# Optimization experiments

Measured on AMD Instinct MI355X. Metric: run time of the kernel, lower is better.

## Reference

```python
import jax, jax.numpy as jnp
import numpy as np

B, T, C, H = 4, 2048, 1024, 16
HD = C // H  # head dim = 64


def setup_inputs() -> dict:
    key = jax.random.key(0)
    k1, k2, k3, k4, k5 = jax.random.split(key, 5)
    s_in = 1.0 / np.sqrt(C)
    return {
        "x": jax.random.normal(k1, (B, T, C), dtype=jnp.float32),
        "W_attn": jax.random.uniform(k2, (C, 3 * C), dtype=jnp.float32, minval=-s_in, maxval=s_in),
        "b_attn": jax.random.uniform(k3, (3 * C,), dtype=jnp.float32, minval=-s_in, maxval=s_in),
        "W_proj": jax.random.uniform(k4, (C, C), dtype=jnp.float32, minval=-s_in, maxval=s_in),
        "b_proj": jax.random.uniform(k5, (C,), dtype=jnp.float32, minval=-s_in, maxval=s_in),
    }


def reference(x, W_attn, b_attn, W_proj, b_proj):
    Bx, Tx, Cx = x.shape
    qkv = x @ W_attn + b_attn                      # [B,T,3C]
    q, k, v = jnp.split(qkv, 3, axis=2)
    # [B,T,C] -> [B,H,T,HD]
    def heads(t):
        return t.reshape(Bx, Tx, H, HD).transpose(0, 2, 1, 3)
    q, k, v = heads(q), heads(k), heads(v)
    scale = 1.0 / np.sqrt(HD).astype(np.float32)
    att = jnp.einsum('bhqd,bhkd->bhqk', q, k) * scale
    causal = jnp.tril(jnp.ones((Tx, Tx), dtype=bool))
    att = jnp.where(causal[None, None], att, -jnp.inf)
    att = jax.nn.softmax(att, axis=-1)
    y = jnp.einsum('bhqk,bhkd->bhqd', att, v)      # [B,H,T,HD]
    y = y.transpose(0, 2, 1, 3).reshape(Bx, Tx, Cx)
    return y @ W_proj + b_proj
```

## Files before the change

kernel.cpp:

```cpp
#include <hip/hip_runtime.h>
#include <math.h>

#define Bn 4
#define Tn 2048
#define Cn 1024
#define Hn 16
#define HDn 64
#define Mn (Bn * Tn)

typedef unsigned short u16;
typedef unsigned int u32;
typedef __attribute__((ext_vector_type(8))) short bf16x8;
typedef __attribute__((ext_vector_type(8))) unsigned short us8;
typedef __attribute__((ext_vector_type(4))) float f32x4;
typedef __attribute__((ext_vector_type(16))) float f32x16;
typedef __attribute__((ext_vector_type(4))) unsigned int u32x4;

__device__ __forceinline__ float b2f(u16 u) {
    return __uint_as_float(((u32)u) << 16);
}
__device__ __forceinline__ u16 f2b(float f) {
    u32 u = __float_as_uint(f);
    return (u16)((u + 0x7FFFu + ((u >> 16) & 1u)) >> 16);
}
__device__ __forceinline__ u32 cvtpk(float a, float b) {
    u32 d;
    asm("v_cvt_pk_bf16_f32 %0, %1, %2" : "=v"(d) : "v"(a), "v"(b));
    return d;
}
__device__ __forceinline__ void pswap(u32& a, u32& b) {
    asm("v_permlane32_swap_b32 %0, %1" : "+v"(a), "+v"(b));
}

__device__ __forceinline__ int xcd_work(int bid, int nwg) {
    return (bid & 7) * (nwg >> 3) + (bid >> 3);
}

#define GLL(srcp, dstp)                                                     \
    __builtin_amdgcn_global_load_lds(                                       \
        (const __attribute__((address_space(1))) u32*)(srcp),               \
        (__attribute__((address_space(3))) u32*)(dstp), 16, 0, 0)

#define WAITCNT6() asm volatile("s_waitcnt vmcnt(6)" ::: "memory")
#define WAITCNT4() asm volatile("s_waitcnt vmcnt(4)" ::: "memory")
#define WAITCNT0() asm volatile("s_waitcnt vmcnt(0)" ::: "memory")

__global__ __launch_bounds__(256) void cvt_f32_bf16_kernel(
    const float4* __restrict__ in, ushort4* __restrict__ out, int n4)
{
    for (int i = blockIdx.x * 256 + threadIdx.x; i < n4; i += gridDim.x * 256) {
        float4 v = in[i];
        ushort4 o;
        o.x = f2b(v.x); o.y = f2b(v.y); o.z = f2b(v.z); o.w = f2b(v.w);
        out[i] = o;
    }
}

__global__ __launch_bounds__(256) void transpose_cvt_kernel(
    const float* __restrict__ in, u16* __restrict__ out, int R, int Cc)
{
    __shared__ u16 t[32][33];
    const int c0 = blockIdx.x * 32, r0 = blockIdx.y * 32;
    const int tx = threadIdx.x & 31, ty = threadIdx.x >> 5;
    #pragma unroll
    for (int i = 0; i < 32; i += 8)
        t[ty + i][tx] = f2b(in[(size_t)(r0 + ty + i) * Cc + c0 + tx]);
    __syncthreads();
    #pragma unroll
    for (int i = 0; i < 32; i += 8)
        out[(size_t)(c0 + ty + i) * R + r0 + tx] = t[tx][ty + i];
}

template <bool OUT_BF16, bool QKV_MODE>
__global__ __launch_bounds__(256, 2) void gemm_bf16_kernel(
    const u16* __restrict__ A, const u16* __restrict__ BT,
    const float* __restrict__ bias,
    u16* __restrict__ outb, float* __restrict__ outf, u16* __restrict__ vTout,
    int N, int K, int nx)
{
    __shared__ u16 Al[3][128 * 32];
    __shared__ u16 Bl[3][256 * 32];

    const int tid = threadIdx.x;
    const int workid = xcd_work(blockIdx.x, gridDim.x);
    const int brow = (workid / nx) * 128;
    const int bcol = (workid % nx) * 256;
    const int w  = tid >> 6;
    const int wr = w >> 1, wc = w & 1;
    const int l  = tid & 63;
    const int lr = l & 15;
    const int lk = (l >> 4) << 3;

    const int sr = l >> 2;
    const int sc = (l & 3) << 3;

    f32x4 acc[4][8];
    #pragma unroll
    for (int m = 0; m < 4; ++m)
        #pragma unroll
        for (int n = 0; n < 8; ++n) acc[m][n] = (f32x4){0.f, 0.f, 0.f, 0.f};

    #define STAGE_G(k0, bufi)                                                   \
        do {                                                                    \
            GLL(&A [(size_t)(brow + 32 * w +      sr) * K + (k0) + sc],         \
                &Al[bufi][(32 * w) * 32]);                                      \
            GLL(&A [(size_t)(brow + 32 * w + 16 + sr) * K + (k0) + sc],         \
                &Al[bufi][(32 * w + 16) * 32]);                                 \
            GLL(&BT[(size_t)(bcol + 64 * w +      sr) * K + (k0) + sc],         \
                &Bl[bufi][(64 * w) * 32]);                                      \
            GLL(&BT[(size_t)(bcol + 64 * w + 16 + sr) * K + (k0) + sc],         \
                &Bl[bufi][(64 * w + 16) * 32]);                                 \
            GLL(&BT[(size_t)(bcol + 64 * w + 32 + sr) * K + (k0) + sc],         \
                &Bl[bufi][(64 * w + 32) * 32]);                                 \
            GLL(&BT[(size_t)(bcol + 64 * w + 48 + sr) * K + (k0) + sc],         \
                &Bl[bufi][(64 * w + 48) * 32]);                                 \
        } while (0)

    const int T = K >> 5;
    STAGE_G(0, 0);
    STAGE_G(32, 1);

    int cur = 0;
    for (int t = 0; t < T; ++t) {
        if (t < T - 1) WAITCNT6();
        else           WAITCNT0();
        __builtin_amdgcn_s_barrier();

        if (t + 2 < T) {
            const int nb = cur + 2 >= 3 ? cur - 1 : cur + 2;
            STAGE_G((t + 2) << 5, nb);
        }

        bf16x8 a[4], b[8];
        #pragma unroll
        for (int m = 0; m < 4; ++m)
            a[m] = *(const bf16x8*)&Al[cur][(wr * 64 + m * 16 + lr) * 32 + lk];
        #pragma unroll
        for (int n = 0; n < 8; ++n)
            b[n] = *(const bf16x8*)&Bl[cur][(wc * 128 + n * 16 + lr) * 32 + lk];

        __builtin_amdgcn_s_setprio(1);
        #pragma unroll
        for (int m = 0; m < 4; ++m)
            #pragma unroll
            for (int n = 0; n < 8; ++n)
                acc[m][n] = __builtin_amdgcn_mfma_f32_16x16x32_bf16(
                    a[m], b[n], acc[m][n], 0, 0, 0);
        __builtin_amdgcn_s_setprio(0);

        cur = cur == 2 ? 0 : cur + 1;
    }
    #undef STAGE_G

    const int orow0 = brow + wr * 64 + ((l >> 4) << 2);
    const int ocol0 = bcol + wc * 128 + lr;
    if (QKV_MODE && bcol >= 2048) {
        #pragma unroll
        for (int n = 0; n < 8; ++n) {
            const int c = ocol0 + n * 16 - 2048;
            const float bv = bias[ocol0 + n * 16];
            #pragma unroll
            for (int m = 0; m < 4; ++m) {
                const int row0 = orow0 + m * 16;
                const int bb = row0 >> 11, t0 = row0 & 2047;
                ushort4 pk;
                pk.x = f2b(acc[m][n][0] + bv);
                pk.y = f2b(acc[m][n][1] + bv);
                pk.z = f2b(acc[m][n][2] + bv);
                pk.w = f2b(acc[m][n][3] + bv);
                *(ushort4*)&vTout[((size_t)bb * Cn + c) * Tn + t0] = pk;
            }
        }
    } else {
        #pragma unroll
        for (int n = 0; n < 8; ++n) {
            const int col = ocol0 + n * 16;
            const float bv = bias[col];
            #pragma unroll
            for (int m = 0; m < 4; ++m) {
                #pragma unroll
                for (int r = 0; r < 4; ++r) {
                    const int row = orow0 + m * 16 + r;
                    const float v = acc[m][n][r] + bv;
                    if (OUT_BF16) outb[(size_t)row * N + col] = f2b(v);
                    else          outf[(size_t)row * N + col] = v;
                }
            }
        }
    }
}

__global__ __launch_bounds__(256, 2) void attn_mfma7_kernel(
    const u16* __restrict__ qkvb, const u16* __restrict__ vT,
    u16* __restrict__ yb)
{
    __shared__ u16 Kb[3][64 * 64];
    __shared__ u16 Vb[3][64 * 64];

    const int tid = threadIdx.x;
    const int w   = tid >> 6;
    const int l   = tid & 63;
    const int q31 = l & 31;
    const int hi  = l >> 5;
    const int work = xcd_work(blockIdx.x, 512);
    const int pr  = work & 7;
    const int bh  = work >> 3;
    const int b   = bh >> 4, h = bh & 15;

    const float S2 = 0.18033688f;

    const u16* Kg = qkvb + (size_t)(b * Tn) * (3 * Cn) + Cn + h * HDn;
    const u16* Vg = vT + (size_t)bh * HDn * Tn;

    const int srow = l >> 3;
    const int schk = ((l & 7) ^ srow) << 3;
    const int rloc = w * 16;
    const int rsw8 = q31 & 7;

    #define STAGE_A(kt, bufi)                                                  \
        do {                                                                   \
            _Pragma("unroll")                                                  \
            for (int jc = 0; jc < 2; ++jc) {                                   \
                const int rr = rloc + jc * 8;                                  \
                GLL(Kg + (size_t)((kt) * 64 + rr + srow) * (3 * Cn) + schk,    \
                    &Kb[bufi][rr * 64]);                                       \
                GLL(Vg + (size_t)(rr + srow) * Tn + (kt) * 64 + schk,          \
                    &Vb[bufi][rr * 64]);                                       \
            }                                                                  \
        } while (0)

    #pragma unroll 1
    for (int half = 0; half < 2; ++half) {
        const int qt = half ? (15 - pr) : pr;
        const int ktmax = 2 * qt + 2;
        const int qrow0 = qt * 128 + w * 32;
        const int qglob = qrow0 + q31;

        const u16* Qp = qkvb + (size_t)(b * Tn + qglob) * (3 * Cn)
                        + h * HDn + hi * 8;
        bf16x8 qf[4];
        #pragma unroll
        for (int c = 0; c < 4; ++c) qf[c] = *(const bf16x8*)(Qp + c * 16);

        f32x16 O0, O1;
        #pragma unroll
        for (int r = 0; r < 16; ++r) { O0[r] = 0.f; O1[r] = 0.f; }
        float m = -INFINITY, ls = 0.f;

        STAGE_A(0, 0);
        STAGE_A(1, 1);

        int cur = 0;
        for (int kt = 0; kt < ktmax; ++kt) {
            if (kt < ktmax - 1) WAITCNT4();
            else                WAITCNT0();
            __builtin_amdgcn_s_barrier();

            if (kt + 2 < ktmax) {
                const int nb = cur + 2 >= 3 ? cur - 1 : cur + 2;
                STAGE_A(kt + 2, nb);
            }
            const u16* Kc = Kb[cur];
            const u16* Vc = Vb[cur];

            if (kt * 64 <= qrow0 + 31) {
                f32x16 S0, S1;
                #pragma unroll
                for (int r = 0; r < 16; ++r) { S0[r] = 0.f; S1[r] = 0.f; }
                __builtin_amdgcn_s_setprio(1);
                #pragma unroll
                for (int c = 0; c < 4; ++c) {
                    const int co = ((2 * c + hi) ^ rsw8) << 3;
                    const bf16x8 k0 = *(const bf16x8*)&Kc[q31 * 64 + co];
                    const bf16x8 k1 = *(const bf16x8*)&Kc[(32 + q31) * 64 + co];
                    S0 = __builtin_amdgcn_mfma_f32_32x32x16_bf16(k0, qf[c], S0, 0, 0, 0);
                    S1 = __builtin_amdgcn_mfma_f32_32x32x16_bf16(k1, qf[c], S1, 0, 0, 0);
                }
                __builtin_amdgcn_s_setprio(0);

                if (kt * 64 + 63 > qrow0) {
                    #pragma unroll
                    for (int r = 0; r < 16; ++r) {
                        const int kl = kt * 64 + (r & 3) + 8 * (r >> 2) + 4 * hi;
                        if (kl > qglob)      S0[r] = -INFINITY;
                        if (kl + 32 > qglob) S1[r] = -INFINITY;
                    }
                }

                float mt = S0[0];
                #pragma unroll
                for (int r = 1; r < 16; ++r) mt = fmaxf(mt, S0[r]);
                #pragma unroll
                for (int r = 0; r < 16; ++r) mt = fmaxf(mt, S1[r]);
                mt = fmaxf(mt, __shfl_xor(mt, 32));

                float lscale = 1.f;
                if (__any(mt > m + 64.f)) {
                    const float mn = fmaxf(m, mt);
                    const float alpha = exp2f((m - mn) * S2);
                    m = mn; lscale = alpha;
                    #pragma unroll
                    for (int r = 0; r < 16; ++r) {
                        const int qloc = (r & 3) + 8 * (r >> 2) + 4 * hi;
                        const float ar = __shfl(alpha, qloc);
                        O0[r] *= ar; O1[r] *= ar;
                    }
                }

                float lt = 0.f;
                u32 w0[8], w1[8];
                #pragma unroll
                for (int i = 0; i < 8; ++i) {
                    const float p0 = exp2f((S0[2 * i]     - m) * S2);
                    const float p1 = exp2f((S0[2 * i + 1] - m) * S2);
                    const float p2 = exp2f((S1[2 * i]     - m) * S2);
                    const float p3 = exp2f((S1[2 * i + 1] - m) * S2);
                    lt += (p0 + p1) + (p2 + p3);
                    w0[i] = cvtpk(p0, p1);
                    w1[i] = cvtpk(p2, p3);
                }
                lt += __shfl_xor(lt, 32);
                ls = ls * lscale + lt;

                __builtin_amdgcn_s_setprio(1);
                #pragma unroll
                for (int t2 = 0; t2 < 2; ++t2) {
                    #pragma unroll
                    for (int c1 = 0; c1 < 2; ++c1) {
                        u32 a0 = t2 ? w1[4 * c1 + 0] : w0[4 * c1 + 0];
                        u32 b0 = t2 ? w1[4 * c1 + 2] : w0[4 * c1 + 2];
                        u32 a1 = t2 ? w1[4 * c1 + 1] : w0[4 * c1 + 1];
                        u32 b1 = t2 ? w1[4 * c1 + 3] : w0[4 * c1 + 3];
                        pswap(a0, b0);
                        pswap(a1, b1);
                        u32x4 fr; fr.x = a0; fr.y = a1; fr.z = b0; fr.w = b1;
                        const bf16x8 pf = __builtin_bit_cast(bf16x8, fr);
                        const int c = t2 * 2 + c1;
                        const int co = ((2 * c + hi) ^ rsw8) << 3;
                        const bf16x8 v0 = *(const bf16x8*)&Vc[q31 * 64 + co];
                        const bf16x8 v1 = *(const bf16x8*)&Vc[(32 + q31) * 64 + co];
                        O0 = __builtin_amdgcn_mfma_f32_32x32x16_bf16(pf, v0, O0, 0, 0, 0);
                        O1 = __builtin_amdgcn_mfma_f32_32x32x16_bf16(pf, v1, O1, 0, 0, 0);
                    }
                }
                __builtin_amdgcn_s_setprio(0);
            }

            cur = cur == 2 ? 0 : cur + 1;
        }

        __builtin_amdgcn_s_barrier();

        #pragma unroll
        for (int r = 0; r < 16; ++r) {
            const int qloc = (r & 3) + 8 * (r >> 2) + 4 * hi;
            const float inv = __builtin_amdgcn_rcpf(__shfl(ls, qloc));
            u16* yp = yb + (size_t)(b * Tn + qrow0 + qloc) * Cn + h * HDn + q31;
            yp[0]  = f2b(O0[r] * inv);
            yp[32] = f2b(O1[r] * inv);
        }
    }
    #undef STAGE_A
}

extern "C" void kernel_launch(void* const* d_in, const int* in_sizes, int n_in,
                              void* d_out, int out_size, void* d_ws, size_t ws_size,
                              hipStream_t stream)
{
    const float* x      = (const float*)d_in[0];
    const float* W_attn = (const float*)d_in[1];
    const float* b_attn = (const float*)d_in[2];
    const float* W_proj = (const float*)d_in[3];
    const float* b_proj = (const float*)d_in[4];
    float* out = (float*)d_out;

    u16* xb   = (u16*)d_ws;
    u16* WaT  = xb   + (size_t)Mn * Cn;
    u16* WpT  = WaT  + (size_t)3 * Cn * Cn;
    u16* qkvb = WpT  + (size_t)Cn * Cn;
    u16* yb   = qkvb + (size_t)Mn * 3 * Cn;
    u16* vT   = yb   + (size_t)Mn * Cn;

    cvt_f32_bf16_kernel<<<2048, 256, 0, stream>>>(
        (const float4*)x, (ushort4*)xb, Mn * Cn / 4);

    transpose_cvt_kernel<<<dim3(3 * Cn / 32, Cn / 32), 256, 0, stream>>>(
        W_attn, WaT, Cn, 3 * Cn);
    transpose_cvt_kernel<<<dim3(Cn / 32, Cn / 32), 256, 0, stream>>>(
        W_proj, WpT, Cn, Cn);

    gemm_bf16_kernel<true, true><<<64 * 12, 256, 0, stream>>>(
        xb, WaT, b_attn, qkvb, nullptr, vT, 3 * Cn, Cn, 12);

    attn_mfma7_kernel<<<512, 256, 0, stream>>>(qkvb, vT, yb);

    gemm_bf16_kernel<false, false><<<64 * 4, 256, 0, stream>>>(
        yb, WpT, b_proj, nullptr, out, nullptr, Cn, Cn, 4);
}
```

Before: 207.1 us.

## Shrink proj GEMM tile to 128x128 and streamline softmax max/exp

The output projection GEMM gets its own kernel with 128x128 tiles. That doubles the grid from 256 to 512 workgroups so all CUs on the device are filled, since the old 256-wide tile left many idle. In the attention kernel, the row max uses v_max3 reductions, exp2 is swapped for the raw hardware builtin with a folded FMA scale, and the row sum is split into two accumulators to shorten dependency chains. The raw exp2 builtin skips denormal handling, which can slightly change tiny values.

```diff
diff --git a/kernel.cpp b/kernel.cpp
--- a/kernel.cpp
+++ b/kernel.cpp
@@ -31,6 +31,12 @@
 __device__ __forceinline__ void pswap(u32& a, u32& b) {
     asm("v_permlane32_swap_b32 %0, %1" : "+v"(a), "+v"(b));
 }
+__device__ __forceinline__ float max3f(float a, float b, float c) {
+    float d;
+    asm("v_max3_f32 %0, %1, %2, %3" : "=v"(d) : "v"(a), "v"(b), "v"(c));
+    return d;
+}
+#define EXP2R(x) __builtin_amdgcn_exp2f(x)
 
 __device__ __forceinline__ int xcd_work(int bid, int nwg) {
     return (bid & 7) * (nwg >> 3) + (bid >> 3);
@@ -71,11 +77,10 @@
         out[(size_t)(c0 + ty + i) * R + r0 + tx] = t[tx][ty + i];
 }
 
-template <bool OUT_BF16, bool QKV_MODE>
-__global__ __launch_bounds__(256, 2) void gemm_bf16_kernel(
+__global__ __launch_bounds__(256, 2) void gemm_qkv_kernel(
     const u16* __restrict__ A, const u16* __restrict__ BT,
     const float* __restrict__ bias,
-    u16* __restrict__ outb, float* __restrict__ outf, u16* __restrict__ vTout,
+    u16* __restrict__ outb, u16* __restrict__ vTout,
     int N, int K, int nx)
 {
     __shared__ u16 Al[3][128 * 32];
@@ -154,7 +159,7 @@
 
     const int orow0 = brow + wr * 64 + ((l >> 4) << 2);
     const int ocol0 = bcol + wc * 128 + lr;
-    if (QKV_MODE && bcol >= 2048) {
+    if (bcol >= 2048) {
         #pragma unroll
         for (int n = 0; n < 8; ++n) {
             const int c = ocol0 + n * 16 - 2048;
@@ -181,16 +186,104 @@
                 #pragma unroll
                 for (int r = 0; r < 4; ++r) {
                     const int row = orow0 + m * 16 + r;
-                    const float v = acc[m][n][r] + bv;
-                    if (OUT_BF16) outb[(size_t)row * N + col] = f2b(v);
-                    else          outf[(size_t)row * N + col] = v;
+                    outb[(size_t)row * N + col] = f2b(acc[m][n][r] + bv);
                 }
             }
         }
     }
 }
 
-__global__ __launch_bounds__(256, 2) void attn_mfma7_kernel(
+__global__ __launch_bounds__(256) void gemm_proj_kernel(
+    const u16* __restrict__ A, const u16* __restrict__ BT,
+    const float* __restrict__ bias, float* __restrict__ outf,
+    int N, int K, int nx)
+{
+    __shared__ u16 Al[3][128 * 32];
+    __shared__ u16 Bl[3][128 * 32];
+
+    const int tid = threadIdx.x;
+    const int workid = xcd_work(blockIdx.x, gridDim.x);
+    const int brow = (workid / nx) * 128;
+    const int bcol = (workid % nx) * 128;
+    const int w  = tid >> 6;
+    const int wr = w >> 1, wc = w & 1;
+    const int l  = tid & 63;
+    const int lr = l & 15;
+    const int lk = (l >> 4) << 3;
+
+    const int r0s = tid >> 2,            c0s = (tid & 3) << 3;
+    const int r1s = (256 + tid) >> 2;
+    const int d0s = (tid & 192) * 8;
+    const int d1s = (256 + (tid & 192)) * 8;
+
+    f32x4 acc[4][4];
+    #pragma unroll
+    for (int m = 0; m < 4; ++m)
+        #pragma unroll
+        for (int n = 0; n < 4; ++n) acc[m][n] = (f32x4){0.f, 0.f, 0.f, 0.f};
+
+    #define STAGE_P(k0, bufi)                                                \
+        do {                                                                 \
+            GLL(&A [(size_t)(brow + r0s) * K + (k0) + c0s], &Al[bufi][d0s]); \
+            GLL(&BT[(size_t)(bcol + r0s) * K + (k0) + c0s], &Bl[bufi][d0s]); \
+            GLL(&A [(size_t)(brow + r1s) * K + (k0) + c0s], &Al[bufi][d1s]); \
+            GLL(&BT[(size_t)(bcol + r1s) * K + (k0) + c0s], &Bl[bufi][d1s]); \
+        } while (0)
+
+    const int T = K >> 5;
+    STAGE_P(0, 0);
+    STAGE_P(32, 1);
+
+    int cur = 0;
+    for (int t = 0; t < T; ++t) {
+        if (t < T - 1) WAITCNT4();
+        else           WAITCNT0();
+        __builtin_amdgcn_s_barrier();
+
+        if (t + 2 < T) {
+            const int nb = cur + 2 >= 3 ? cur - 1 : cur + 2;
+            STAGE_P((t + 2) << 5, nb);
+        }
+
+        bf16x8 a[4], b[4];
+        #pragma unroll
+        for (int m = 0; m < 4; ++m)
+            a[m] = *(const bf16x8*)&Al[cur][(wr * 64 + m * 16 + lr) * 32 + lk];
+        #pragma unroll
+        for (int n = 0; n < 4; ++n)
+            b[n] = *(const bf16x8*)&Bl[cur][(wc * 64 + n * 16 + lr) * 32 + lk];
+
+        __builtin_amdgcn_s_setprio(1);
+        #pragma unroll
+        for (int m = 0; m < 4; ++m)
+            #pragma unroll
+            for (int n = 0; n < 4; ++n)
+                acc[m][n] = __builtin_amdgcn_mfma_f32_16x16x32_bf16(
+                    a[m], b[n], acc[m][n], 0, 0, 0);
+        __builtin_amdgcn_s_setprio(0);
+
+        cur = cur == 2 ? 0 : cur + 1;
+    }
+    #undef STAGE_P
+
+    const int orow0 = brow + wr * 64 + ((l >> 4) << 2);
+    const int ocol0 = bcol + wc * 64 + lr;
+    #pragma unroll
+    for (int n = 0; n < 4; ++n) {
+        const int col = ocol0 + n * 16;
+        const float bv = bias[col];
+        #pragma unroll
+        for (int m = 0; m < 4; ++m) {
+            #pragma unroll
+            for (int r = 0; r < 4; ++r) {
+                const int row = orow0 + m * 16 + r;
+                outf[(size_t)row * N + col] = acc[m][n][r] + bv;
+            }
+        }
+    }
+}
+
+__global__ __launch_bounds__(256, 2) void attn_mfma8_kernel(
     const u16* __restrict__ qkvb, const u16* __restrict__ vT,
     u16* __restrict__ yb)
 {
@@ -287,17 +380,28 @@
                     }
                 }
 
-                float mt = S0[0];
-                #pragma unroll
-                for (int r = 1; r < 16; ++r) mt = fmaxf(mt, S0[r]);
-                #pragma unroll
-                for (int r = 0; r < 16; ++r) mt = fmaxf(mt, S1[r]);
+                float a0 = max3f(S0[0],  S0[1],  S0[2]);
+                float a1 = max3f(S0[3],  S0[4],  S0[5]);
+                float a2 = max3f(S0[6],  S0[7],  S0[8]);
+                float a3 = max3f(S0[9],  S0[10], S0[11]);
+                float a4 = max3f(S0[12], S0[13], S0[14]);
+                float a5 = max3f(S0[15], S1[0],  S1[1]);
+                float a6 = max3f(S1[2],  S1[3],  S1[4]);
+                float a7 = max3f(S1[5],  S1[6],  S1[7]);
+                float a8 = max3f(S1[8],  S1[9],  S1[10]);
+                float a9 = max3f(S1[11], S1[12], S1[13]);
+                float aA = fmaxf(S1[14], S1[15]);
+                float b0 = max3f(a0, a1, a2);
+                float b1 = max3f(a3, a4, a5);
+                float b2 = max3f(a6, a7, a8);
+                float b3 = fmaxf(a9, aA);
+                float mt = fmaxf(fmaxf(b0, b1), fmaxf(b2, b3));
                 mt = fmaxf(mt, __shfl_xor(mt, 32));
 
                 float lscale = 1.f;
                 if (__any(mt > m + 64.f)) {
                     const float mn = fmaxf(m, mt);
-                    const float alpha = exp2f((m - mn) * S2);
+                    const float alpha = EXP2R((m - mn) * S2);
                     m = mn; lscale = alpha;
                     #pragma unroll
                     for (int r = 0; r < 16; ++r) {
@@ -307,18 +411,21 @@
                     }
                 }
 
-                float lt = 0.f;
+                const float nms2 = -m * S2;
+                float lt0 = 0.f, lt1 = 0.f;
                 u32 w0[8], w1[8];
                 #pragma unroll
                 for (int i = 0; i < 8; ++i) {
-                    const float p0 = exp2f((S0[2 * i]     - m) * S2);
-                    const float p1 = exp2f((S0[2 * i + 1] - m) * S2);
-                    const float p2 = exp2f((S1[2 * i]     - m) * S2);
-                    const float p3 = exp2f((S1[2 * i + 1] - m) * S2);
-                    lt += (p0 + p1) + (p2 + p3);
+                    const float p0 = EXP2R(fmaf(S0[2 * i],     S2, nms2));
+                    const float p1 = EXP2R(fmaf(S0[2 * i + 1], S2, nms2));
+                    const float p2 = EXP2R(fmaf(S1[2 * i],     S2, nms2));
+                    const float p3 = EXP2R(fmaf(S1[2 * i + 1], S2, nms2));
+                    lt0 += (p0 + p1);
+                    lt1 += (p2 + p3);
                     w0[i] = cvtpk(p0, p1);
                     w1[i] = cvtpk(p2, p3);
                 }
+                float lt = lt0 + lt1;
                 lt += __shfl_xor(lt, 32);
                 ls = ls * lscale + lt;
 
@@ -327,13 +434,13 @@
                 for (int t2 = 0; t2 < 2; ++t2) {
                     #pragma unroll
                     for (int c1 = 0; c1 < 2; ++c1) {
-                        u32 a0 = t2 ? w1[4 * c1 + 0] : w0[4 * c1 + 0];
-                        u32 b0 = t2 ? w1[4 * c1 + 2] : w0[4 * c1 + 2];
-                        u32 a1 = t2 ? w1[4 * c1 + 1] : w0[4 * c1 + 1];
-                        u32 b1 = t2 ? w1[4 * c1 + 3] : w0[4 * c1 + 3];
-                        pswap(a0, b0);
-                        pswap(a1, b1);
-                        u32x4 fr; fr.x = a0; fr.y = a1; fr.z = b0; fr.w = b1;
+                        u32 a0w = t2 ? w1[4 * c1 + 0] : w0[4 * c1 + 0];
+                        u32 b0w = t2 ? w1[4 * c1 + 2] : w0[4 * c1 + 2];
+                        u32 a1w = t2 ? w1[4 * c1 + 1] : w0[4 * c1 + 1];
+                        u32 b1w = t2 ? w1[4 * c1 + 3] : w0[4 * c1 + 3];
+                        pswap(a0w, b0w);
+                        pswap(a1w, b1w);
+                        u32x4 fr; fr.x = a0w; fr.y = a1w; fr.z = b0w; fr.w = b1w;
                         const bf16x8 pf = __builtin_bit_cast(bf16x8, fr);
                         const int c = t2 * 2 + c1;
                         const int co = ((2 * c + hi) ^ rsw8) << 3;
@@ -389,11 +496,11 @@
     transpose_cvt_kernel<<<dim3(Cn / 32, Cn / 32), 256, 0, stream>>>(
         W_proj, WpT, Cn, Cn);
 
-    gemm_bf16_kernel<true, true><<<64 * 12, 256, 0, stream>>>(
-        xb, WaT, b_attn, qkvb, nullptr, vT, 3 * Cn, Cn, 12);
-
-    attn_mfma7_kernel<<<512, 256, 0, stream>>>(qkvb, vT, yb);
-
-    gemm_bf16_kernel<false, false><<<64 * 4, 256, 0, stream>>>(
-        yb, WpT, b_proj, nullptr, out, nullptr, Cn, Cn, 4);
-}
+    gemm_qkv_kernel<<<64 * 12, 256, 0, stream>>>(
+        xb, WaT, b_attn, qkvb, vT, 3 * Cn, Cn, 12);
+
+    attn_mfma8_kernel<<<512, 256, 0, stream>>>(qkvb, vT, yb);
+
+    gemm_proj_kernel<<<8 * 64, 256, 0, stream>>>(
+        yb, WpT, b_proj, out, Cn, Cn, 8);
+}
```

New measurement: 178.7 us. 13.8% less time.
